# Performance work log

Hardware: AMD Instinct MI355X
Metric: run time of the kernel (lower is better)

Reference implementation:

```python
import jax, jax.numpy as jnp
import numpy as np

B, H, S, D = 8, 16, 1024, 64


def setup_inputs() -> dict:
    key = jax.random.key(0)
    kq, kk, kv, km = jax.random.split(key, 4)
    Q = jax.random.normal(kq, (B, H, S, D), dtype=jnp.float32)
    K = jax.random.normal(kk, (B, H, S, D), dtype=jnp.float32)
    V = jax.random.normal(kv, (B, H, S, D), dtype=jnp.float32)
    attn_mask = jax.random.randint(km, (B, H, S, S), 0, 2).astype(jnp.bool_)
    return {"Q": Q, "K": K, "V": V, "attn_mask": attn_mask}


def reference(Q, K, V, attn_mask):
    d_k = Q.shape[-1]
    scale = 1.0 / np.sqrt(d_k).astype(np.float32)
    # scores: [B, H, S, S]
    scores = jnp.einsum("bhqd,bhkd->bhqk", Q, K) * scale
    scores = jnp.where(attn_mask, jnp.float32(-1e9), scores)
    attn = jax.nn.softmax(scores, axis=-1)
    context = jnp.einsum("bhqk,bhkd->bhqd", attn, V)
    return context, attn
```

## Files before the change

kernel.cpp:

```cpp
#include <hip/hip_runtime.h>

#define S_ 1024
#define D_ 64
#define CTX_ELEMS (8 * 16 * 1024 * 64)

__global__ void detect_mask_kernel(const unsigned int* __restrict__ mask,
                                   int* __restrict__ flag) {
  const int t = threadIdx.x;
  if (t == 0) flag[0] = 0;
  __syncthreads();
  unsigned int local = 0;
  for (int i = t; i < 1024; i += 256) {
    unsigned int w = mask[i];
    if (w == 0x3F800000u)      local |= 2u;
    else if (w > 1u)           local |= 1u;
  }
  if (local) atomicOr(flag, (int)local);
}

__global__ __launch_bounds__(256, 2)
void attn_fused_kernel(const float* __restrict__ Q, const float* __restrict__ K,
                       const float* __restrict__ V, const void* __restrict__ mask,
                       float* __restrict__ out, const int* __restrict__ flag) {
  __shared__ float4 Qs[16][17];
  __shared__ float4 KVs[128][17];
  __shared__ float  As[16][132];

  const int t  = threadIdx.x;
  const int qt = blockIdx.x;
  const int bh = blockIdx.y;
  const int q0 = qt * 16;

  const int qg = t >> 6;
  const int kl = t & 63;

  const float* Qb = Q + (size_t)bh * (S_ * D_) + (size_t)q0 * D_;
  const float* Kb = K + (size_t)bh * (S_ * D_);
  const float* Vb = V + (size_t)bh * (S_ * D_);

  {
    const int r = t >> 4, c = t & 15;
    Qs[r][c] = ((const float4*)Qb)[r * 16 + c];
  }

  float acc[4][16];
#pragma unroll
  for (int qq = 0; qq < 4; ++qq)
#pragma unroll
    for (int ci = 0; ci < 16; ++ci) acc[qq][ci] = 0.f;

#pragma unroll
  for (int kt = 0; kt < 8; ++kt) {
    __syncthreads();
#pragma unroll
    for (int i = 0; i < 8; ++i) {
      const int fi = t + 256 * i;
      KVs[fi >> 4][fi & 15] = ((const float4*)Kb)[kt * 2048 + fi];
    }
    __syncthreads();
#pragma unroll
    for (int d4 = 0; d4 < 16; ++d4) {
      const float4 kv0 = KVs[kl][d4];
      const float4 kv1 = KVs[kl + 64][d4];
#pragma unroll
      for (int qq = 0; qq < 4; ++qq) {
        const float4 qv = Qs[4 * qg + qq][d4];
        acc[qq][2 * kt]     += qv.x * kv0.x + qv.y * kv0.y + qv.z * kv0.z + qv.w * kv0.w;
        acc[qq][2 * kt + 1] += qv.x * kv1.x + qv.y * kv1.y + qv.z * kv1.z + qv.w * kv1.w;
      }
    }
  }

  const float scale = 0.125f;
  const int mode = *flag;
  const size_t mbase = (size_t)bh * ((size_t)S_ * S_) + (size_t)q0 * S_;
  if (mode & 2) {
    const float* mf = (const float*)mask + mbase;
#pragma unroll
    for (int qq = 0; qq < 4; ++qq) {
      const float* mr = mf + (4 * qg + qq) * S_ + kl;
#pragma unroll
      for (int ci = 0; ci < 16; ++ci)
        acc[qq][ci] = (mr[64 * ci] != 0.f) ? -1e9f : acc[qq][ci] * scale;
    }
  } else if (mode & 1) {
    const unsigned char* mu = (const unsigned char*)mask + mbase;
#pragma unroll
    for (int qq = 0; qq < 4; ++qq) {
      const unsigned char* mr = mu + (4 * qg + qq) * S_ + kl;
#pragma unroll
      for (int ci = 0; ci < 16; ++ci)
        acc[qq][ci] = mr[64 * ci] ? -1e9f : acc[qq][ci] * scale;
    }
  } else {
    const int* mi = (const int*)mask + mbase;
#pragma unroll
    for (int qq = 0; qq < 4; ++qq) {
      const int* mr = mi + (4 * qg + qq) * S_ + kl;
#pragma unroll
      for (int ci = 0; ci < 16; ++ci)
        acc[qq][ci] = mr[64 * ci] ? -1e9f : acc[qq][ci] * scale;
    }
  }

  float* outAttn = out + CTX_ELEMS;
#pragma unroll
  for (int qq = 0; qq < 4; ++qq) {
    float mx = -3.4e38f;
#pragma unroll
    for (int ci = 0; ci < 16; ++ci) mx = fmaxf(mx, acc[qq][ci]);
#pragma unroll
    for (int off = 32; off > 0; off >>= 1) mx = fmaxf(mx, __shfl_xor(mx, off, 64));
    float sum = 0.f;
#pragma unroll
    for (int ci = 0; ci < 16; ++ci) {
      const float p = __expf(acc[qq][ci] - mx);
      acc[qq][ci] = p;
      sum += p;
    }
#pragma unroll
    for (int off = 32; off > 0; off >>= 1) sum += __shfl_xor(sum, off, 64);
    const float inv = 1.0f / sum;
#pragma unroll
    for (int ci = 0; ci < 16; ++ci) acc[qq][ci] *= inv;
    float* ar = outAttn + mbase + (size_t)(4 * qg + qq) * S_ + kl;
#pragma unroll
    for (int ci = 0; ci < 16; ++ci) ar[64 * ci] = acc[qq][ci];
  }

  const int qB = t >> 4, d4B = t & 15;
  float4 c4 = {0.f, 0.f, 0.f, 0.f};
#pragma unroll
  for (int vt = 0; vt < 8; ++vt) {
    __syncthreads();
#pragma unroll
    for (int i = 0; i < 8; ++i) {
      const int fi = t + 256 * i;
      KVs[fi >> 4][fi & 15] = ((const float4*)Vb)[vt * 2048 + fi];
    }
#pragma unroll
    for (int qq = 0; qq < 4; ++qq) {
      As[4 * qg + qq][kl]      = acc[qq][2 * vt];
      As[4 * qg + qq][kl + 64] = acc[qq][2 * vt + 1];
    }
    __syncthreads();
#pragma unroll 16
    for (int k_local = 0; k_local < 128; ++k_local) {
      const float  a  = As[qB][k_local];
      const float4 vv = KVs[k_local][d4B];
      c4.x += a * vv.x; c4.y += a * vv.y; c4.z += a * vv.z; c4.w += a * vv.w;
    }
  }
  ((float4*)(out + (size_t)bh * (S_ * D_) + (size_t)(q0 + qB) * D_))[d4B] = c4;
}

extern "C" void kernel_launch(void* const* d_in, const int* in_sizes, int n_in,
                              void* d_out, int out_size, void* d_ws, size_t ws_size,
                              hipStream_t stream) {
  const float* Q = (const float*)d_in[0];
  const float* K = (const float*)d_in[1];
  const float* V = (const float*)d_in[2];
  const void* mask = d_in[3];
  int* flag = (int*)d_ws;

  detect_mask_kernel<<<1, 256, 0, stream>>>((const unsigned int*)mask, flag);

  dim3 grid(S_ / 16, 8 * 16);
  attn_fused_kernel<<<grid, 256, 0, stream>>>(Q, K, V, mask, (float*)d_out, flag);
}
```

Measured before the change: 1.587 ms.

## Double query tile per block, prefetch K/V into registers, remap blocks per XCD

Each block now handles 32 query rows instead of 16, which halves how often K and V are reloaded from global memory across the grid. K/V tiles are prefetched into registers for the next iteration while the current tile is being computed, overlapping global loads with math. The grid becomes 1D and is remapped so that all query tiles of one (batch, head) land on the same XCD, which should improve L2 reuse of K and V. The cost is much higher register pressure (acc grows to 8x16, plus 8 float4 staging registers) under launch_bounds(256,2), which could cause spills and fewer blocks.

```diff
diff --git a/kernel.cpp b/kernel.cpp
--- a/kernel.cpp
+++ b/kernel.cpp
@@ -22,32 +22,42 @@
 void attn_fused_kernel(const float* __restrict__ Q, const float* __restrict__ K,
                        const float* __restrict__ V, const void* __restrict__ mask,
                        float* __restrict__ out, const int* __restrict__ flag) {
-  __shared__ float4 Qs[16][17];
+  __shared__ float4 Qs[32][17];
   __shared__ float4 KVs[128][17];
-  __shared__ float  As[16][132];
+  __shared__ float  As[32][132];
 
-  const int t  = threadIdx.x;
-  const int qt = blockIdx.x;
-  const int bh = blockIdx.y;
-  const int q0 = qt * 16;
+  const int t = threadIdx.x;
+  const int id   = blockIdx.x;
+  const int xcd  = id & 7;
+  const int slot = id >> 3;
+  const int bh   = xcd + 8 * (slot >> 5);
+  const int qt   = slot & 31;
+  const int q0   = qt * 32;
 
   const int qg = t >> 6;
   const int kl = t & 63;
 
   const float* Qb = Q + (size_t)bh * (S_ * D_) + (size_t)q0 * D_;
-  const float* Kb = K + (size_t)bh * (S_ * D_);
-  const float* Vb = V + (size_t)bh * (S_ * D_);
+  const float4* Kb4 = (const float4*)(K + (size_t)bh * (S_ * D_));
+  const float4* Vb4 = (const float4*)(V + (size_t)bh * (S_ * D_));
 
   {
-    const int r = t >> 4, c = t & 15;
-    Qs[r][c] = ((const float4*)Qb)[r * 16 + c];
+#pragma unroll
+    for (int i = 0; i < 2; ++i) {
+      const int fi = t + 256 * i;
+      Qs[fi >> 4][fi & 15] = ((const float4*)Qb)[fi];
+    }
   }
 
-  float acc[4][16];
+  float acc[8][16];
 #pragma unroll
-  for (int qq = 0; qq < 4; ++qq)
+  for (int qq = 0; qq < 8; ++qq)
 #pragma unroll
     for (int ci = 0; ci < 16; ++ci) acc[qq][ci] = 0.f;
+
+  float4 st[8];
+#pragma unroll
+  for (int i = 0; i < 8; ++i) st[i] = Kb4[t + 256 * i];
 
 #pragma unroll
   for (int kt = 0; kt < 8; ++kt) {
@@ -55,7 +65,14 @@
 #pragma unroll
     for (int i = 0; i < 8; ++i) {
       const int fi = t + 256 * i;
-      KVs[fi >> 4][fi & 15] = ((const float4*)Kb)[kt * 2048 + fi];
+      KVs[fi >> 4][fi & 15] = st[i];
+    }
+    if (kt < 7) {
+#pragma unroll
+      for (int i = 0; i < 8; ++i) st[i] = Kb4[(kt + 1) * 2048 + t + 256 * i];
+    } else {
+#pragma unroll
+      for (int i = 0; i < 8; ++i) st[i] = Vb4[t + 256 * i];
     }
     __syncthreads();
 #pragma unroll
@@ -63,8 +80,8 @@
       const float4 kv0 = KVs[kl][d4];
       const float4 kv1 = KVs[kl + 64][d4];
 #pragma unroll
-      for (int qq = 0; qq < 4; ++qq) {
-        const float4 qv = Qs[4 * qg + qq][d4];
+      for (int qq = 0; qq < 8; ++qq) {
+        const float4 qv = Qs[8 * qg + qq][d4];
         acc[qq][2 * kt]     += qv.x * kv0.x + qv.y * kv0.y + qv.z * kv0.z + qv.w * kv0.w;
         acc[qq][2 * kt + 1] += qv.x * kv1.x + qv.y * kv1.y + qv.z * kv1.z + qv.w * kv1.w;
       }
@@ -77,8 +94,8 @@
   if (mode & 2) {
     const float* mf = (const float*)mask + mbase;
 #pragma unroll
-    for (int qq = 0; qq < 4; ++qq) {
-      const float* mr = mf + (4 * qg + qq) * S_ + kl;
+    for (int qq = 0; qq < 8; ++qq) {
+      const float* mr = mf + (8 * qg + qq) * S_ + kl;
 #pragma unroll
       for (int ci = 0; ci < 16; ++ci)
         acc[qq][ci] = (mr[64 * ci] != 0.f) ? -1e9f : acc[qq][ci] * scale;
@@ -86,8 +103,8 @@
   } else if (mode & 1) {
     const unsigned char* mu = (const unsigned char*)mask + mbase;
 #pragma unroll
-    for (int qq = 0; qq < 4; ++qq) {
-      const unsigned char* mr = mu + (4 * qg + qq) * S_ + kl;
+    for (int qq = 0; qq < 8; ++qq) {
+      const unsigned char* mr = mu + (8 * qg + qq) * S_ + kl;
 #pragma unroll
       for (int ci = 0; ci < 16; ++ci)
         acc[qq][ci] = mr[64 * ci] ? -1e9f : acc[qq][ci] * scale;
@@ -95,8 +112,8 @@
   } else {
     const int* mi = (const int*)mask + mbase;
 #pragma unroll
-    for (int qq = 0; qq < 4; ++qq) {
-      const int* mr = mi + (4 * qg + qq) * S_ + kl;
+    for (int qq = 0; qq < 8; ++qq) {
+      const int* mr = mi + (8 * qg + qq) * S_ + kl;
 #pragma unroll
       for (int ci = 0; ci < 16; ++ci)
         acc[qq][ci] = mr[64 * ci] ? -1e9f : acc[qq][ci] * scale;
@@ -105,7 +122,7 @@
 
   float* outAttn = out + CTX_ELEMS;
 #pragma unroll
-  for (int qq = 0; qq < 4; ++qq) {
+  for (int qq = 0; qq < 8; ++qq) {
     float mx = -3.4e38f;
 #pragma unroll
     for (int ci = 0; ci < 16; ++ci) mx = fmaxf(mx, acc[qq][ci]);
@@ -123,35 +140,44 @@
     const float inv = 1.0f / sum;
 #pragma unroll
     for (int ci = 0; ci < 16; ++ci) acc[qq][ci] *= inv;
-    float* ar = outAttn + mbase + (size_t)(4 * qg + qq) * S_ + kl;
+    float* ar = outAttn + mbase + (size_t)(8 * qg + qq) * S_ + kl;
 #pragma unroll
     for (int ci = 0; ci < 16; ++ci) ar[64 * ci] = acc[qq][ci];
   }
 
   const int qB = t >> 4, d4B = t & 15;
-  float4 c4 = {0.f, 0.f, 0.f, 0.f};
+  float4 c0 = {0.f, 0.f, 0.f, 0.f};
+  float4 c1 = {0.f, 0.f, 0.f, 0.f};
 #pragma unroll
   for (int vt = 0; vt < 8; ++vt) {
     __syncthreads();
 #pragma unroll
     for (int i = 0; i < 8; ++i) {
       const int fi = t + 256 * i;
-      KVs[fi >> 4][fi & 15] = ((const float4*)Vb)[vt * 2048 + fi];
+      KVs[fi >> 4][fi & 15] = st[i];
+    }
+    if (vt < 7) {
+#pragma unroll
+      for (int i = 0; i < 8; ++i) st[i] = Vb4[(vt + 1) * 2048 + t + 256 * i];
     }
 #pragma unroll
-    for (int qq = 0; qq < 4; ++qq) {
-      As[4 * qg + qq][kl]      = acc[qq][2 * vt];
-      As[4 * qg + qq][kl + 64] = acc[qq][2 * vt + 1];
+    for (int qq = 0; qq < 8; ++qq) {
+      As[8 * qg + qq][kl]      = acc[qq][2 * vt];
+      As[8 * qg + qq][kl + 64] = acc[qq][2 * vt + 1];
     }
     __syncthreads();
 #pragma unroll 16
     for (int k_local = 0; k_local < 128; ++k_local) {
-      const float  a  = As[qB][k_local];
+      const float  a0 = As[qB][k_local];
+      const float  a1 = As[qB + 16][k_local];
       const float4 vv = KVs[k_local][d4B];
-      c4.x += a * vv.x; c4.y += a * vv.y; c4.z += a * vv.z; c4.w += a * vv.w;
+      c0.x += a0 * vv.x; c0.y += a0 * vv.y; c0.z += a0 * vv.z; c0.w += a0 * vv.w;
+      c1.x += a1 * vv.x; c1.y += a1 * vv.y; c1.z += a1 * vv.z; c1.w += a1 * vv.w;
     }
   }
-  ((float4*)(out + (size_t)bh * (S_ * D_) + (size_t)(q0 + qB) * D_))[d4B] = c4;
+  float* ctx = out + (size_t)bh * (S_ * D_);
+  ((float4*)(ctx + (size_t)(q0 + qB) * D_))[d4B]      = c0;
+  ((float4*)(ctx + (size_t)(q0 + qB + 16) * D_))[d4B] = c1;
 }
 
 extern "C" void kernel_launch(void* const* d_in, const int* in_sizes, int n_in,
@@ -165,6 +191,6 @@
 
   detect_mask_kernel<<<1, 256, 0, stream>>>((const unsigned int*)mask, flag);
 
-  dim3 grid(S_ / 16, 8 * 16);
+  dim3 grid(32 * 128);
   attn_fused_kernel<<<grid, 256, 0, stream>>>(Q, K, V, mask, (float*)d_out, flag);
 }
```

Result: slower. 1.814 ms (+14.3%).

## Double-buffer K/V tiles with async global-to-LDS loads and XCD-aware block mapping

Applied to the files above, without the earlier changes.

Replaces the synchronous K/V staging with double-buffered 64-row tiles loaded through global_load_lds, using an XOR swizzle to avoid LDS bank conflicts. Q is now read directly from global memory instead of LDS. Blocks are remapped so all blocks of one head land on the same XCD, which is meant to improve L2 reuse of K/V. The PV product is restructured with a transposed probability tile and a cross-lane shuffle reduction, and attention writes are interleaved with the PV loop. Occupancy is raised to four blocks per CU, at the cost of more complex synchronization and of relying on the async-load builtin.

```diff
diff --git a/kernel.cpp b/kernel.cpp
--- a/kernel.cpp
+++ b/kernel.cpp
@@ -18,30 +18,53 @@
   if (local) atomicOr(flag, (int)local);
 }
 
-__global__ __launch_bounds__(256, 2)
+__device__ __forceinline__ void async_ld16(const float4* g, float* lds) {
+  __builtin_amdgcn_global_load_lds(
+      (const __attribute__((address_space(1))) void*)g,
+      (__attribute__((address_space(3))) void*)lds, 16, 0, 0);
+}
+
+__global__ __launch_bounds__(256, 4)
 void attn_fused_kernel(const float* __restrict__ Q, const float* __restrict__ K,
                        const float* __restrict__ V, const void* __restrict__ mask,
                        float* __restrict__ out, const int* __restrict__ flag) {
-  __shared__ float4 Qs[16][17];
-  __shared__ float4 KVs[128][17];
-  __shared__ float  As[16][132];
+  __shared__ float KV[2][64][64];
+  __shared__ float AsT[64][20];
 
   const int t  = threadIdx.x;
-  const int qt = blockIdx.x;
-  const int bh = blockIdx.y;
-  const int q0 = qt * 16;
-
-  const int qg = t >> 6;
-  const int kl = t & 63;
-
-  const float* Qb = Q + (size_t)bh * (S_ * D_) + (size_t)q0 * D_;
-  const float* Kb = K + (size_t)bh * (S_ * D_);
-  const float* Vb = V + (size_t)bh * (S_ * D_);
-
+  const int id = blockIdx.x;
+  const int xcd  = id & 7;
+  const int slot = id >> 3;
+  const int bh   = xcd + 8 * (slot >> 6);
+  const int qt   = slot & 63;
+  const int q0   = qt * 16;
+
+  const int w = t >> 6;
+  const int l = t & 63;
+
+  const float4* Kb4 = (const float4*)(K + (size_t)bh * (S_ * D_));
+  const float4* Vb4 = (const float4*)(V + (size_t)bh * (S_ * D_));
+
+  const float* Qrow[4];
   {
-    const int r = t >> 4, c = t & 15;
-    Qs[r][c] = ((const float4*)Qb)[r * 16 + c];
-  }
+    const int wu = __builtin_amdgcn_readfirstlane(w);
+#pragma unroll
+    for (int qq = 0; qq < 4; ++qq)
+      Qrow[qq] = Q + (size_t)bh * (S_ * D_) + (size_t)(q0 + 4 * wu + qq) * D_;
+  }
+
+#define STAGE(src4, tile, buf)                                               \
+  {                                                                          \
+    _Pragma("unroll")                                                        \
+    for (int j = 0; j < 4; ++j) {                                            \
+      const int rr = (4 * w + j) * 4 + (l >> 4);                             \
+      const int cc = (l & 15) ^ (rr & 7);                                    \
+      async_ld16((src4) + ((size_t)((tile) * 64 + rr) * 16 + cc),            \
+                 &KV[buf][0][0] + (4 * w + j) * 256);                        \
+    }                                                                        \
+  }
+
+  STAGE(Kb4, 0, 0);
 
   float acc[4][16];
 #pragma unroll
@@ -49,26 +72,22 @@
 #pragma unroll
     for (int ci = 0; ci < 16; ++ci) acc[qq][ci] = 0.f;
 
-#pragma unroll
-  for (int kt = 0; kt < 8; ++kt) {
+  __syncthreads();
+
+#pragma unroll
+  for (int kt = 0; kt < 16; ++kt) {
+    if (kt < 15) { STAGE(Kb4, kt + 1, (kt + 1) & 1); }
+    else         { STAGE(Vb4, 0, 0); }
+#pragma unroll 4
+    for (int d4 = 0; d4 < 16; ++d4) {
+      const float4 kv = *(const float4*)&KV[kt & 1][l][(d4 ^ (l & 7)) << 2];
+#pragma unroll
+      for (int qq = 0; qq < 4; ++qq) {
+        const float4 qv = *(const float4*)(Qrow[qq] + (d4 << 2));
+        acc[qq][kt] += qv.x * kv.x + qv.y * kv.y + qv.z * kv.z + qv.w * kv.w;
+      }
+    }
     __syncthreads();
-#pragma unroll
-    for (int i = 0; i < 8; ++i) {
-      const int fi = t + 256 * i;
-      KVs[fi >> 4][fi & 15] = ((const float4*)Kb)[kt * 2048 + fi];
-    }
-    __syncthreads();
-#pragma unroll
-    for (int d4 = 0; d4 < 16; ++d4) {
-      const float4 kv0 = KVs[kl][d4];
-      const float4 kv1 = KVs[kl + 64][d4];
-#pragma unroll
-      for (int qq = 0; qq < 4; ++qq) {
-        const float4 qv = Qs[4 * qg + qq][d4];
-        acc[qq][2 * kt]     += qv.x * kv0.x + qv.y * kv0.y + qv.z * kv0.z + qv.w * kv0.w;
-        acc[qq][2 * kt + 1] += qv.x * kv1.x + qv.y * kv1.y + qv.z * kv1.z + qv.w * kv1.w;
-      }
-    }
   }
 
   const float scale = 0.125f;
@@ -78,7 +97,7 @@
     const float* mf = (const float*)mask + mbase;
 #pragma unroll
     for (int qq = 0; qq < 4; ++qq) {
-      const float* mr = mf + (4 * qg + qq) * S_ + kl;
+      const float* mr = mf + (4 * w + qq) * S_ + l;
 #pragma unroll
       for (int ci = 0; ci < 16; ++ci)
         acc[qq][ci] = (mr[64 * ci] != 0.f) ? -1e9f : acc[qq][ci] * scale;
@@ -87,7 +106,7 @@
     const unsigned char* mu = (const unsigned char*)mask + mbase;
 #pragma unroll
     for (int qq = 0; qq < 4; ++qq) {
-      const unsigned char* mr = mu + (4 * qg + qq) * S_ + kl;
+      const unsigned char* mr = mu + (4 * w + qq) * S_ + l;
 #pragma unroll
       for (int ci = 0; ci < 16; ++ci)
         acc[qq][ci] = mr[64 * ci] ? -1e9f : acc[qq][ci] * scale;
@@ -96,14 +115,13 @@
     const int* mi = (const int*)mask + mbase;
 #pragma unroll
     for (int qq = 0; qq < 4; ++qq) {
-      const int* mr = mi + (4 * qg + qq) * S_ + kl;
+      const int* mr = mi + (4 * w + qq) * S_ + l;
 #pragma unroll
       for (int ci = 0; ci < 16; ++ci)
         acc[qq][ci] = mr[64 * ci] ? -1e9f : acc[qq][ci] * scale;
     }
   }
 
-  float* outAttn = out + CTX_ELEMS;
 #pragma unroll
   for (int qq = 0; qq < 4; ++qq) {
     float mx = -3.4e38f;
@@ -123,35 +141,54 @@
     const float inv = 1.0f / sum;
 #pragma unroll
     for (int ci = 0; ci < 16; ++ci) acc[qq][ci] *= inv;
-    float* ar = outAttn + mbase + (size_t)(4 * qg + qq) * S_ + kl;
-#pragma unroll
-    for (int ci = 0; ci < 16; ++ci) ar[64 * ci] = acc[qq][ci];
-  }
-
-  const int qB = t >> 4, d4B = t & 15;
-  float4 c4 = {0.f, 0.f, 0.f, 0.f};
-#pragma unroll
-  for (int vt = 0; vt < 8; ++vt) {
+  }
+
+  float* outAttn = out + CTX_ELEMS;
+  const int d4B = l & 15;
+  const int kg  = l >> 4;
+  float4 cacc[4];
+#pragma unroll
+  for (int qq = 0; qq < 4; ++qq) { cacc[qq].x = cacc[qq].y = cacc[qq].z = cacc[qq].w = 0.f; }
+
+#pragma unroll
+  for (int vt = 0; vt < 16; ++vt) {
+    if (vt < 15) { STAGE(Vb4, vt + 1, (vt + 1) & 1); }
+#pragma unroll
+    for (int qq = 0; qq < 4; ++qq) {
+      AsT[l][4 * w + qq] = acc[qq][vt];
+      outAttn[mbase + (size_t)(4 * w + qq) * S_ + vt * 64 + l] = acc[qq][vt];
+    }
+#pragma unroll 4
+    for (int kc = 0; kc < 16; ++kc) {
+      const int krow = kc * 4 + kg;
+      const float4 av = *(const float4*)&AsT[krow][4 * w];
+      const float4 vv = *(const float4*)&KV[vt & 1][krow][(d4B ^ (krow & 7)) << 2];
+      cacc[0].x += av.x * vv.x; cacc[0].y += av.x * vv.y; cacc[0].z += av.x * vv.z; cacc[0].w += av.x * vv.w;
+      cacc[1].x += av.y * vv.x; cacc[1].y += av.y * vv.y; cacc[1].z += av.y * vv.z; cacc[1].w += av.y * vv.w;
+      cacc[2].x += av.z * vv.x; cacc[2].y += av.z * vv.y; cacc[2].z += av.z * vv.z; cacc[2].w += av.z * vv.w;
+      cacc[3].x += av.w * vv.x; cacc[3].y += av.w * vv.y; cacc[3].z += av.w * vv.z; cacc[3].w += av.w * vv.w;
+    }
     __syncthreads();
-#pragma unroll
-    for (int i = 0; i < 8; ++i) {
-      const int fi = t + 256 * i;
-      KVs[fi >> 4][fi & 15] = ((const float4*)Vb)[vt * 2048 + fi];
-    }
-#pragma unroll
-    for (int qq = 0; qq < 4; ++qq) {
-      As[4 * qg + qq][kl]      = acc[qq][2 * vt];
-      As[4 * qg + qq][kl + 64] = acc[qq][2 * vt + 1];
-    }
-    __syncthreads();
-#pragma unroll 16
-    for (int k_local = 0; k_local < 128; ++k_local) {
-      const float  a  = As[qB][k_local];
-      const float4 vv = KVs[k_local][d4B];
-      c4.x += a * vv.x; c4.y += a * vv.y; c4.z += a * vv.z; c4.w += a * vv.w;
-    }
-  }
-  ((float4*)(out + (size_t)bh * (S_ * D_) + (size_t)(q0 + qB) * D_))[d4B] = c4;
+  }
+
+#pragma unroll
+  for (int qq = 0; qq < 4; ++qq) {
+    cacc[qq].x += __shfl_xor(cacc[qq].x, 16, 64);
+    cacc[qq].y += __shfl_xor(cacc[qq].y, 16, 64);
+    cacc[qq].z += __shfl_xor(cacc[qq].z, 16, 64);
+    cacc[qq].w += __shfl_xor(cacc[qq].w, 16, 64);
+    cacc[qq].x += __shfl_xor(cacc[qq].x, 32, 64);
+    cacc[qq].y += __shfl_xor(cacc[qq].y, 32, 64);
+    cacc[qq].z += __shfl_xor(cacc[qq].z, 32, 64);
+    cacc[qq].w += __shfl_xor(cacc[qq].w, 32, 64);
+  }
+  if (l < 16) {
+    float* ctx = out + (size_t)bh * (S_ * D_);
+#pragma unroll
+    for (int qq = 0; qq < 4; ++qq)
+      ((float4*)(ctx + (size_t)(q0 + 4 * w + qq) * D_))[l] = cacc[qq];
+  }
+#undef STAGE
 }
 
 extern "C" void kernel_launch(void* const* d_in, const int* in_sizes, int n_in,
@@ -165,6 +202,6 @@
 
   detect_mask_kernel<<<1, 256, 0, stream>>>((const unsigned int*)mask, flag);
 
-  dim3 grid(S_ / 16, 8 * 16);
+  dim3 grid(64 * 128);
   attn_fused_kernel<<<grid, 256, 0, stream>>>(Q, K, V, mask, (float*)d_out, flag);
 }
```

New measurement: 1.874 ms. 1.18x slower.
